# Optimization experiments

Measured on AMD Instinct MI355X. Metric: run time of the kernel, lower is better.

The kernel has to match this reference:

```python
import jax, jax.numpy as jnp
import numpy as np

N, E, D = 50000, 800000, 128   # nodes, edges, input feat dim
H, C = 4, 32                   # heads, per-head channels (H*C = 128)
OUT = 128                      # final linear out_channels
NEG_SLOPE = 0.2


def _glorot(k, shape):
    fan = shape[0] + shape[-1]
    return jax.random.normal(k, shape, jnp.float32) * np.float32(np.sqrt(2.0 / fan))


def setup_inputs() -> dict:
    key = jax.random.key(0)
    ks = jax.random.split(key, 16)
    HC = H * C
    z = lambda n: jnp.zeros((n,), jnp.float32)
    return {
        "x": jax.random.normal(ks[0], (N, D), jnp.float32),
        "edge_index": jax.random.randint(ks[1], (2, E), 0, N),
        "edge_attr": jax.random.uniform(ks[2], (E, 1), jnp.float32),
        # GATv2 layer 1 (in = D)
        "Wl1": _glorot(ks[3], (D, HC)), "bl1": z(HC),
        "Wr1": _glorot(ks[4], (D, HC)), "br1": z(HC),
        "We1": _glorot(ks[5], (1, HC)),
        "att1": _glorot(ks[6], (H, C)),
        "bo1": z(HC),
        # GATv2 layer 2 (in = H*C)
        "Wl2": _glorot(ks[7], (HC, HC)), "bl2": z(HC),
        "Wr2": _glorot(ks[8], (HC, HC)), "br2": z(HC),
        "We2": _glorot(ks[9], (1, HC)),
        "att2": _glorot(ks[10], (H, C)),
        "bo2": z(HC),
        # final Linear
        "Wlin": _glorot(ks[11], (HC, OUT)), "blin": z(OUT),
    }


def _segment_softmax(logits, seg, n):
    # logits: [E_tot, H], seg: [E_tot] target node ids
    m = jax.ops.segment_max(logits, seg, num_segments=n)          # [N, H]
    m = jnp.where(jnp.isfinite(m), m, 0.0)                         # empty-segment guard
    e = jnp.exp(logits - m[seg])
    s = jax.ops.segment_sum(e, seg, num_segments=n)                # [N, H]
    return e / (s[seg] + 1e-16)


def _gatv2_layer(x, src, dst, eattr, Wl, bl, Wr, br, We, att, bo):
    n = x.shape[0]
    xl = (x @ Wl + bl).reshape(n, H, C)   # source transform (lin_l)
    xr = (x @ Wr + br).reshape(n, H, C)   # target transform (lin_r)
    ee = (eattr @ We).reshape(-1, H, C)   # edge transform (lin_edge)
    m = jax.nn.leaky_relu(xl[src] + xr[dst] + ee, NEG_SLOPE)       # [E_tot, H, C]
    logits = jnp.einsum('ehc,hc->eh', m, att)                      # [E_tot, H]
    alpha = _segment_softmax(logits, dst, n)                       # [E_tot, H]
    out = jax.ops.segment_sum(xl[src] * alpha[..., None], dst, num_segments=n)
    return out.reshape(n, H * C) + bo


def _with_self_loops(edge_index, edge_attr, n):
    # PyG add_self_loops(fill_value='mean'): loop attr = mean of incoming edge attrs
    src, dst = edge_index[0], edge_index[1]
    sums = jax.ops.segment_sum(edge_attr, dst, num_segments=n)     # [N, 1]
    cnts = jax.ops.segment_sum(jnp.ones((edge_attr.shape[0], 1), edge_attr.dtype),
                               dst, num_segments=n)
    loop_attr = jnp.where(cnts > 0, sums / jnp.maximum(cnts, 1.0), 0.0)
    ar = jnp.arange(n, dtype=src.dtype)
    full_src = jnp.concatenate([src, ar])
    full_dst = jnp.concatenate([dst, ar])
    full_attr = jnp.concatenate([edge_attr, loop_attr], axis=0)
    return full_src, full_dst, full_attr


def reference(x, edge_index, edge_attr,
              Wl1, bl1, Wr1, br1, We1, att1, bo1,
              Wl2, bl2, Wr2, br2, We2, att2, bo2,
              Wlin, blin):
    x = x.astype(jnp.float32)
    edge_attr = edge_attr.astype(jnp.float32)
    src, dst, eattr = _with_self_loops(edge_index, edge_attr, x.shape[0])
    h = jax.nn.relu(_gatv2_layer(x, src, dst, eattr, Wl1, bl1, Wr1, br1, We1, att1, bo1))
    h = jax.nn.relu(_gatv2_layer(h, src, dst, eattr, Wl2, bl2, Wr2, br2, We2, att2, bo2))
    return jax.nn.relu(h @ Wlin + blin)
```

## Files before the change

kernel.cpp:

```cpp
#include <hip/hip_runtime.h>
#include <hip/hip_fp16.h>
#include <math.h>

#define NEG 0.2f
#define CNT_SHIFT 42
#define SUM_MASK ((1ULL << CNT_SHIFT) - 1)
#define ROWS 48

typedef _Float16 hf2 __attribute__((ext_vector_type(2)));
typedef _Float16 hf8 __attribute__((ext_vector_type(8)));
typedef float f4 __attribute__((ext_vector_type(4)));

template <int CTRL>
__device__ __forceinline__ float dpp_radd(float x) {
  int t = __builtin_amdgcn_update_dpp(0, __float_as_int(x), CTRL, 0xf, 0xf,
                                      false);
  return x + __int_as_float(t);
}

__device__ __forceinline__ uint4 pack_wline(const float* __restrict__ W,
                                            int L) {
  int lane = L & 63, nt = (L >> 6) & 7, kc = L >> 9;
  int kbase = kc * 32 + (lane >> 4) * 8;
  int col = nt * 16 + (lane & 15);
  const float* wp = W + (size_t)kbase * 128 + col;
  uint4 pk;
  pk.x = __builtin_bit_cast(unsigned, __builtin_amdgcn_cvt_pkrtz(wp[0], wp[128]));
  pk.y = __builtin_bit_cast(unsigned, __builtin_amdgcn_cvt_pkrtz(wp[256], wp[384]));
  pk.z = __builtin_bit_cast(unsigned, __builtin_amdgcn_cvt_pkrtz(wp[512], wp[640]));
  pk.w = __builtin_bit_cast(unsigned, __builtin_amdgcn_cvt_pkrtz(wp[768], wp[896]));
  return pk;
}

__global__ __launch_bounds__(256, 2) void k_fuse1(
    const float* __restrict__ X, const float* __restrict__ Wa,
    const float* __restrict__ Wb, const float* __restrict__ Ba,
    const float* __restrict__ Bb, hf2* __restrict__ Y0, hf2* __restrict__ Y1,
    int nrows, int gGemm, const int* __restrict__ ei,
    const float* __restrict__ eattr, unsigned long long* __restrict__ hist,
    unsigned* __restrict__ edge, int E, int nbP,
    const float* __restrict__ W2a, const float* __restrict__ W2b,
    const float* __restrict__ W2c, uint4* __restrict__ wout) {
  __shared__ uint4 Wl[2][1024];
  int bid = blockIdx.x, tid = threadIdx.x;

  if (bid < gGemm) {
    int lane = tid & 63, wid = tid >> 6;
    int quad = lane >> 4, rl = lane & 15;
    int rbase = bid * 128 + wid * 32;

    hf8 a[4][2];
#pragma unroll
    for (int rs = 0; rs < 2; ++rs) {
      int gr = rbase + rs * 16 + rl;
      gr = gr < nrows ? gr : nrows - 1;
      const float* xp = X + (size_t)gr * 128 + quad * 8;
#pragma unroll
      for (int kc = 0; kc < 4; ++kc) {
        float4 u = *reinterpret_cast<const float4*>(xp + kc * 32);
        float4 u2 = *reinterpret_cast<const float4*>(xp + kc * 32 + 4);
        uint4 pk;
        pk.x = __builtin_bit_cast(unsigned, __builtin_amdgcn_cvt_pkrtz(u.x, u.y));
        pk.y = __builtin_bit_cast(unsigned, __builtin_amdgcn_cvt_pkrtz(u.z, u.w));
        pk.z = __builtin_bit_cast(unsigned, __builtin_amdgcn_cvt_pkrtz(u2.x, u2.y));
        pk.w = __builtin_bit_cast(unsigned, __builtin_amdgcn_cvt_pkrtz(u2.z, u2.w));
        a[kc][rs] = __builtin_bit_cast(hf8, pk);
      }
    }

    f4 acc[2][2][8];
#pragma unroll
    for (int m = 0; m < 2; ++m)
#pragma unroll
      for (int rs = 0; rs < 2; ++rs)
#pragma unroll
        for (int nt = 0; nt < 8; ++nt) acc[m][rs][nt] = (f4)0.f;

#pragma unroll
    for (int h = 0; h < 2; ++h) {
      __syncthreads();
#pragma unroll
      for (int m = 0; m < 2; ++m) {
        const float* W = m ? Wb : Wa;
        for (int i = tid; i < 1024; i += 256)
          Wl[m][i] = pack_wline(W, h * 1024 + i);
      }
      __syncthreads();
#pragma unroll
      for (int kcl = 0; kcl < 2; ++kcl) {
        int kc = h * 2 + kcl;
#pragma unroll
        for (int nt = 0; nt < 8; ++nt) {
#pragma unroll
          for (int m = 0; m < 2; ++m) {
            hf8 w = __builtin_bit_cast(hf8,
                Wl[m][(kcl * 8 + nt) * 64 + lane]);
            acc[m][0][nt] = __builtin_amdgcn_mfma_f32_16x16x32_f16(
                w, a[kc][0], acc[m][0][nt], 0, 0, 0);
            acc[m][1][nt] = __builtin_amdgcn_mfma_f32_16x16x32_f16(
                w, a[kc][1], acc[m][1][nt], 0, 0, 0);
          }
        }
      }
    }

#pragma unroll
    for (int m = 0; m < 2; ++m) {
      const float* Bb_ = m ? Bb : Ba;
      hf2* Yv = m ? Y1 : Y0;
#pragma unroll
      for (int rs = 0; rs < 2; ++rs) {
        int row = rbase + rs * 16 + rl;
        if (row < nrows) {
#pragma unroll
          for (int nt = 0; nt < 8; ++nt) {
            f4 av = acc[m][rs][nt];
            int col = nt * 16 + quad * 4;
            float4 bb = *reinterpret_cast<const float4*>(&Bb_[col]);
            float o0 = av[0] + bb.x, o1 = av[1] + bb.y;
            float o2 = av[2] + bb.z, o3 = av[3] + bb.w;
            unsigned p0 = __builtin_bit_cast(unsigned,
                __builtin_amdgcn_cvt_pkrtz(o0, o1));
            unsigned p1 = __builtin_bit_cast(unsigned,
                __builtin_amdgcn_cvt_pkrtz(o2, o3));
            *reinterpret_cast<uint2*>((_Float16*)Yv + (size_t)row * 128 + col)
                = make_uint2(p0, p1);
          }
        }
      }
    }
  } else if (bid < gGemm + nbP) {
    int e0 = (bid - gGemm) * 4096 + tid;
    int d[16], s[16];
    float ea[16];
    bool valid[16];
#pragma unroll
    for (int j = 0; j < 16; ++j) {
      int e = e0 + j * 256;
      valid[j] = e < E;
      int ec = valid[j] ? e : 0;
      d[j] = ei[E + ec];
      s[j] = ei[ec];
      ea[j] = eattr[ec];
    }
#pragma unroll
    for (int j = 0; j < 16; ++j) {
      if (valid[j]) {
        unsigned long long fx =
            (unsigned long long)(ea[j] * 4294967296.0f);
        unsigned long long old =
            atomicAdd(&hist[d[j]], (1ULL << CNT_SHIFT) + fx);
        int rank = (int)(old >> CNT_SHIFT);
        _Float16 h = (_Float16)ea[j];
        unsigned hb = (unsigned)__builtin_bit_cast(unsigned short, h);
        if (rank < ROWS)
          edge[(size_t)d[j] * ROWS + rank] = (unsigned)s[j] | (hb << 16);
      }
    }
  } else {
    int gid = (bid - gGemm - nbP) * 256 + tid;
    if (gid < 3 * 2048) {
      int mat = gid >> 11;
      const float* W = mat == 0 ? W2a : mat == 1 ? W2b : W2c;
      wout[gid] = pack_wline(W, gid & 2047);
    }
  }
}

template <int NMAT, int HALF_OUT>
__global__ __launch_bounds__(256, 2) void k_gemm3(
    const _Float16* __restrict__ X, const uint4* __restrict__ Wp0,
    const uint4* __restrict__ Wp1, const float* __restrict__ B0,
    const float* __restrict__ B1, void* __restrict__ Y0v,
    void* __restrict__ Y1v, int nrows, int dorelu) {
  __shared__ uint4 Wl[NMAT * 2048];
  int tid = threadIdx.x;
  for (int i = tid; i < 2048; i += 256) Wl[i] = Wp0[i];
  if (NMAT == 2)
    for (int i = tid; i < 2048; i += 256) Wl[2048 + i] = Wp1[i];

  int lane = tid & 63, wid = tid >> 6;
  int quad = lane >> 4, rl = lane & 15;
  int rbase = blockIdx.x * 128 + wid * 32;

  hf8 a[4][2];
#pragma unroll
  for (int rs = 0; rs < 2; ++rs) {
    int gr = rbase + rs * 16 + rl;
    gr = gr < nrows ? gr : nrows - 1;
    const _Float16* xp = X + (size_t)gr * 128 + quad * 8;
#pragma unroll
    for (int kc = 0; kc < 4; ++kc)
      a[kc][rs] = *reinterpret_cast<const hf8*>(xp + kc * 32);
  }

  f4 acc[NMAT][2][8];
#pragma unroll
  for (int m = 0; m < NMAT; ++m)
#pragma unroll
    for (int rs = 0; rs < 2; ++rs)
#pragma unroll
      for (int nt = 0; nt < 8; ++nt) acc[m][rs][nt] = (f4)0.f;

  __syncthreads();

#pragma unroll
  for (int kc = 0; kc < 4; ++kc) {
#pragma unroll
    for (int nt = 0; nt < 8; ++nt) {
#pragma unroll
      for (int m = 0; m < NMAT; ++m) {
        hf8 w = __builtin_bit_cast(hf8,
            Wl[m * 2048 + (kc * 8 + nt) * 64 + lane]);
        acc[m][0][nt] = __builtin_amdgcn_mfma_f32_16x16x32_f16(
            w, a[kc][0], acc[m][0][nt], 0, 0, 0);
        acc[m][1][nt] = __builtin_amdgcn_mfma_f32_16x16x32_f16(
            w, a[kc][1], acc[m][1][nt], 0, 0, 0);
      }
    }
  }

#pragma unroll
  for (int m = 0; m < NMAT; ++m) {
    const float* Bb = m ? B1 : B0;
    void* Yv = m ? Y1v : Y0v;
#pragma unroll
    for (int rs = 0; rs < 2; ++rs) {
      int row = rbase + rs * 16 + rl;
      if (row < nrows) {
#pragma unroll
        for (int nt = 0; nt < 8; ++nt) {
          f4 av = acc[m][rs][nt];
          int col = nt * 16 + quad * 4;
          float4 bb = *reinterpret_cast<const float4*>(&Bb[col]);
          float o0 = av[0] + bb.x, o1 = av[1] + bb.y;
          float o2 = av[2] + bb.z, o3 = av[3] + bb.w;
          if (dorelu) {
            o0 = fmaxf(o0, 0.f); o1 = fmaxf(o1, 0.f);
            o2 = fmaxf(o2, 0.f); o3 = fmaxf(o3, 0.f);
          }
          if (HALF_OUT) {
            unsigned p0 = __builtin_bit_cast(unsigned,
                __builtin_amdgcn_cvt_pkrtz(o0, o1));
            unsigned p1 = __builtin_bit_cast(unsigned,
                __builtin_amdgcn_cvt_pkrtz(o2, o3));
            *reinterpret_cast<uint2*>((_Float16*)Yv + (size_t)row * 128 + col)
                = make_uint2(p0, p1);
          } else {
            *reinterpret_cast<float4*>((float*)Yv + (size_t)row * 128 + col)
                = make_float4(o0, o1, o2, o3);
          }
        }
      }
    }
  }
}

__global__ __launch_bounds__(256) void k_gat(const hf2* __restrict__ xl,
    const hf2* __restrict__ xr, const unsigned* __restrict__ edge,
    const unsigned long long* __restrict__ hist, const float* __restrict__ We,
    const float* __restrict__ att, const float* __restrict__ bo,
    hf2* __restrict__ out, int n) {
  int lane = threadIdx.x & 63;
  int wid = threadIdx.x >> 6;
  int v = blockIdx.x * 4 + wid;
  if (v >= n) return;
  int ch = lane * 2;
  hf2 weh = {(_Float16)We[ch], (_Float16)We[ch + 1]};
  hf2 atth = {(_Float16)(att[ch] * 1.44269504f),
              (_Float16)(att[ch + 1] * 1.44269504f)};
  hf2 negh = {(_Float16)NEG, (_Float16)NEG};
  hf2 xrh = xr[(size_t)v * 64 + lane];
  unsigned long long hv = hist[v];
  int cnt = (int)(hv >> CNT_SHIFT);
  int cntc = cnt < ROWS ? cnt : ROWS;
  const unsigned* erow = edge + (size_t)v * ROWS;

  float denom[2] = {0.f, 0.f};
  float ac0[2] = {0.f, 0.f}, ac1[2] = {0.f, 0.f};

  int full = cntc & ~7;
  for (int ofs = 0; ofs < full; ofs += 8) {
    const unsigned* ep = erow + ofs;
    unsigned rec[8];
#pragma unroll
    for (int j = 0; j < 8; ++j) rec[j] = ep[j];
    hf2 xv[8];
#pragma unroll
    for (int j = 0; j < 8; ++j)
      xv[j] = xl[(size_t)(rec[j] & 0xffffu) * 64 + lane];
    float p[8];
#pragma unroll
    for (int j = 0; j < 8; ++j) {
      hf2 eah = __builtin_bit_cast(hf2, (rec[j] >> 16) * 0x10001u);
      hf2 t = (xv[j] + xrh) + eah * weh;
      hf2 tn = t * negh;
      t = __builtin_elementwise_max(t, tn);
      p[j] = __builtin_amdgcn_fdot2(t, atth, 0.f, false);
    }
#pragma unroll
    for (int j = 0; j < 8; ++j) {
      p[j] = dpp_radd<0xB1>(p[j]);
      p[j] = dpp_radd<0x4E>(p[j]);
      p[j] = dpp_radd<0x141>(p[j]);
      p[j] = dpp_radd<0x140>(p[j]);
    }
#pragma unroll
    for (int j = 0; j < 8; ++j) {
      float w = __builtin_amdgcn_exp2f(p[j]);
      denom[j & 1] += w;
      ac0[j & 1] = fmaf(w, (float)xv[j].x, ac0[j & 1]);
      ac1[j & 1] = fmaf(w, (float)xv[j].y, ac1[j & 1]);
    }
  }
  if (full < cntc) {
    const unsigned* ep = erow + full;
    unsigned rec[8];
#pragma unroll
    for (int j = 0; j < 8; ++j) rec[j] = ep[j];
    hf2 xv[8];
#pragma unroll
    for (int j = 0; j < 8; ++j) {
      unsigned si = rec[j] & 0xffffu;
      si = si < (unsigned)n ? si : 0u;
      xv[j] = xl[(size_t)si * 64 + lane];
    }
    float p[8];
#pragma unroll
    for (int j = 0; j < 8; ++j) {
      hf2 eah = __builtin_bit_cast(hf2, (rec[j] >> 16) * 0x10001u);
      hf2 t = (xv[j] + xrh) + eah * weh;
      hf2 tn = t * negh;
      t = __builtin_elementwise_max(t, tn);
      p[j] = __builtin_amdgcn_fdot2(t, atth, 0.f, false);
    }
#pragma unroll
    for (int j = 0; j < 8; ++j) {
      p[j] = dpp_radd<0xB1>(p[j]);
      p[j] = dpp_radd<0x4E>(p[j]);
      p[j] = dpp_radd<0x141>(p[j]);
      p[j] = dpp_radd<0x140>(p[j]);
    }
#pragma unroll
    for (int j = 0; j < 8; ++j) {
      float w = (full + j < cntc) ? __builtin_amdgcn_exp2f(p[j]) : 0.f;
      denom[j & 1] += w;
      ac0[j & 1] = fmaf(w, (float)xv[j].x, ac0[j & 1]);
      ac1[j & 1] = fmaf(w, (float)xv[j].y, ac1[j & 1]);
    }
  }
  {
    float sumf = (float)(hv & SUM_MASK) * 2.3283064365386963e-10f;
    float mean = cnt > 0 ? sumf / (float)cnt : 0.f;
    hf2 xself = xl[(size_t)v * 64 + lane];
    _Float16 mh = (_Float16)mean;
    hf2 meanh = {mh, mh};
    hf2 t = (xself + xrh) + meanh * weh;
    hf2 tn = t * negh;
    t = __builtin_elementwise_max(t, tn);
    float ps = __builtin_amdgcn_fdot2(t, atth, 0.f, false);
    ps = dpp_radd<0xB1>(ps);
    ps = dpp_radd<0x4E>(ps);
    ps = dpp_radd<0x141>(ps);
    ps = dpp_radd<0x140>(ps);
    float w = __builtin_amdgcn_exp2f(ps);
    denom[0] += w;
    ac0[0] = fmaf(w, (float)xself.x, ac0[0]);
    ac1[0] = fmaf(w, (float)xself.y, ac1[0]);
  }
  float rden = 1.0f / (denom[0] + denom[1] + 1e-16f);
  float o0 = fmaxf(fmaf(ac0[0] + ac0[1], rden, bo[ch]), 0.f);
  float o1 = fmaxf(fmaf(ac1[0] + ac1[1], rden, bo[ch + 1]), 0.f);
  hf2 oh = {(_Float16)o0, (_Float16)o1};
  out[(size_t)v * 64 + lane] = oh;
}

extern "C" void kernel_launch(void* const* d_in, const int* in_sizes, int n_in,
                              void* d_out, int out_size, void* d_ws, size_t ws_size,
                              hipStream_t stream) {
  const float* x     = (const float*)d_in[0];
  const int*   ei    = (const int*)d_in[1];
  const float* eattr = (const float*)d_in[2];
  const float* Wl1 = (const float*)d_in[3];
  const float* bl1 = (const float*)d_in[4];
  const float* Wr1 = (const float*)d_in[5];
  const float* br1 = (const float*)d_in[6];
  const float* We1 = (const float*)d_in[7];
  const float* att1 = (const float*)d_in[8];
  const float* bo1 = (const float*)d_in[9];
  const float* Wl2 = (const float*)d_in[10];
  const float* bl2 = (const float*)d_in[11];
  const float* Wr2 = (const float*)d_in[12];
  const float* br2 = (const float*)d_in[13];
  const float* We2 = (const float*)d_in[14];
  const float* att2 = (const float*)d_in[15];
  const float* bo2 = (const float*)d_in[16];
  const float* Wlin = (const float*)d_in[17];
  const float* blin = (const float*)d_in[18];
  float* out = (float*)d_out;

  const int N = in_sizes[0] / 128;
  const int E = in_sizes[1] / 2;

  hf2* xl = (hf2*)d_ws;
  hf2* xr = xl + (size_t)N * 64;
  hf2* h16 = xr + (size_t)N * 64;
  uint4* w16 = (uint4*)(h16 + (size_t)N * 64);
  unsigned long long* hist = (unsigned long long*)(w16 + 3 * 2048);
  unsigned* edge = (unsigned*)(hist + N);

  (void)hipMemsetAsync(hist, 0, sizeof(unsigned long long) * (size_t)N,
                       stream);

  int gGemm = (N + 127) / 128;
  int nbP = (E + 4095) / 4096;
  int gGat = (N + 3) / 4;

  k_fuse1<<<gGemm + nbP + 24, 256, 0, stream>>>(x, Wl1, Wr1, bl1, br1,
      xl, xr, N, gGemm, ei, eattr, hist, edge, E, nbP,
      Wl2, Wr2, Wlin, w16);

  k_gat<<<gGat, 256, 0, stream>>>(xl, xr, edge, hist, We1, att1, bo1, h16, N);

  k_gemm3<2, 1><<<gGemm, 256, 0, stream>>>((const _Float16*)h16,
      w16, w16 + 2048, bl2, br2, xl, xr, N, 0);

  k_gat<<<gGat, 256, 0, stream>>>(xl, xr, edge, hist, We2, att2, bo2, h16, N);

  k_gemm3<1, 0><<<gGemm, 256, 0, stream>>>((const _Float16*)h16,
      w16 + 2 * 2048, nullptr, blin, nullptr, out, nullptr, N, 1);
}
```

Baseline: 276.4 us.

## Distribute edge bucketing via atomic work-stealing chunks across all fused blocks

Measured after the change: 283.0 us. 1.02x slower.

```diff
diff --git a/kernel.cpp b/kernel.cpp
--- a/kernel.cpp
+++ b/kernel.cpp
@@ -38,9 +38,9 @@
     const float* __restrict__ Bb, hf2* __restrict__ Y0, hf2* __restrict__ Y1,
     int nrows, int gGemm, const int* __restrict__ ei,
     const float* __restrict__ eattr, unsigned long long* __restrict__ hist,
-    unsigned* __restrict__ edge, int E, int nbP,
-    const float* __restrict__ W2a, const float* __restrict__ W2b,
-    const float* __restrict__ W2c, uint4* __restrict__ wout) {
+    unsigned* __restrict__ edge, int E, int* __restrict__ cursor,
+    int nChunks, const float* __restrict__ W2a, const float* __restrict__ W2b,
+    const float* __restrict__ W2c, uint4* __restrict__ wout, int nbW) {
   __shared__ uint4 Wl[2][1024];
   int bid = blockIdx.x, tid = threadIdx.x;
 
@@ -129,13 +129,28 @@
         }
       }
     }
-  } else if (bid < gGemm + nbP) {
-    int e0 = (bid - gGemm) * 4096 + tid;
-    int d[16], s[16];
-    float ea[16];
-    bool valid[16];
-#pragma unroll
-    for (int j = 0; j < 16; ++j) {
+  } else if (bid < gGemm + nbW) {
+    int gid = (bid - gGemm) * 256 + tid;
+    if (gid < 3 * 2048) {
+      int mat = gid >> 11;
+      const float* W = mat == 0 ? W2a : mat == 1 ? W2b : W2c;
+      wout[gid] = pack_wline(W, gid & 2047);
+    }
+  }
+
+  for (;;) {
+    __shared__ int chunk_s;
+    if (tid == 0) chunk_s = atomicAdd(cursor, 1);
+    __syncthreads();
+    int chunk = chunk_s;
+    __syncthreads();
+    if (chunk >= nChunks) break;
+    int e0 = chunk * 1024 + tid;
+    int d[4], s[4];
+    float ea[4];
+    bool valid[4];
+#pragma unroll
+    for (int j = 0; j < 4; ++j) {
       int e = e0 + j * 256;
       valid[j] = e < E;
       int ec = valid[j] ? e : 0;
@@ -144,7 +159,7 @@
       ea[j] = eattr[ec];
     }
 #pragma unroll
-    for (int j = 0; j < 16; ++j) {
+    for (int j = 0; j < 4; ++j) {
       if (valid[j]) {
         unsigned long long fx =
             (unsigned long long)(ea[j] * 4294967296.0f);
@@ -156,13 +171,6 @@
         if (rank < ROWS)
           edge[(size_t)d[j] * ROWS + rank] = (unsigned)s[j] | (hb << 16);
       }
-    }
-  } else {
-    int gid = (bid - gGemm - nbP) * 256 + tid;
-    if (gid < 3 * 2048) {
-      int mat = gid >> 11;
-      const float* W = mat == 0 ? W2a : mat == 1 ? W2b : W2c;
-      wout[gid] = pack_wline(W, gid & 2047);
     }
   }
 }
@@ -407,18 +415,21 @@
   hf2* h16 = xr + (size_t)N * 64;
   uint4* w16 = (uint4*)(h16 + (size_t)N * 64);
   unsigned long long* hist = (unsigned long long*)(w16 + 3 * 2048);
-  unsigned* edge = (unsigned*)(hist + N);
-
-  (void)hipMemsetAsync(hist, 0, sizeof(unsigned long long) * (size_t)N,
-                       stream);
+  int* cursor = (int*)(hist + N);
+  unsigned* edge = (unsigned*)(cursor + 4);
+
+  (void)hipMemsetAsync(hist, 0,
+                       sizeof(unsigned long long) * (size_t)N + 16, stream);
 
   int gGemm = (N + 127) / 128;
-  int nbP = (E + 4095) / 4096;
+  int nbW = 24;
+  int nChunks = (E + 1023) / 1024;
+  int nbExtra = 200;
   int gGat = (N + 3) / 4;
 
-  k_fuse1<<<gGemm + nbP + 24, 256, 0, stream>>>(x, Wl1, Wr1, bl1, br1,
-      xl, xr, N, gGemm, ei, eattr, hist, edge, E, nbP,
-      Wl2, Wr2, Wlin, w16);
+  k_fuse1<<<gGemm + nbW + nbExtra, 256, 0, stream>>>(x, Wl1, Wr1, bl1, br1,
+      xl, xr, N, gGemm, ei, eattr, hist, edge, E, cursor, nChunks,
+      Wl2, Wr2, Wlin, w16, nbW);
 
   k_gat<<<gGat, 256, 0, stream>>>(xl, xr, edge, hist, We1, att1, bo1, h16, N);
 
```

## Fuse layer-1 GAT aggregation with layer-2 linear transforms in one kernel

Applied to the files above, without the earlier changes.

New measurement: 271.1 us. Within noise of the previous version (-1.9%).

```diff
diff --git a/kernel.cpp b/kernel.cpp
--- a/kernel.cpp
+++ b/kernel.cpp
@@ -32,244 +32,11 @@
   return pk;
 }
 
-__global__ __launch_bounds__(256, 2) void k_fuse1(
-    const float* __restrict__ X, const float* __restrict__ Wa,
-    const float* __restrict__ Wb, const float* __restrict__ Ba,
-    const float* __restrict__ Bb, hf2* __restrict__ Y0, hf2* __restrict__ Y1,
-    int nrows, int gGemm, const int* __restrict__ ei,
-    const float* __restrict__ eattr, unsigned long long* __restrict__ hist,
-    unsigned* __restrict__ edge, int E, int nbP,
-    const float* __restrict__ W2a, const float* __restrict__ W2b,
-    const float* __restrict__ W2c, uint4* __restrict__ wout) {
-  __shared__ uint4 Wl[2][1024];
-  int bid = blockIdx.x, tid = threadIdx.x;
-
-  if (bid < gGemm) {
-    int lane = tid & 63, wid = tid >> 6;
-    int quad = lane >> 4, rl = lane & 15;
-    int rbase = bid * 128 + wid * 32;
-
-    hf8 a[4][2];
-#pragma unroll
-    for (int rs = 0; rs < 2; ++rs) {
-      int gr = rbase + rs * 16 + rl;
-      gr = gr < nrows ? gr : nrows - 1;
-      const float* xp = X + (size_t)gr * 128 + quad * 8;
-#pragma unroll
-      for (int kc = 0; kc < 4; ++kc) {
-        float4 u = *reinterpret_cast<const float4*>(xp + kc * 32);
-        float4 u2 = *reinterpret_cast<const float4*>(xp + kc * 32 + 4);
-        uint4 pk;
-        pk.x = __builtin_bit_cast(unsigned, __builtin_amdgcn_cvt_pkrtz(u.x, u.y));
-        pk.y = __builtin_bit_cast(unsigned, __builtin_amdgcn_cvt_pkrtz(u.z, u.w));
-        pk.z = __builtin_bit_cast(unsigned, __builtin_amdgcn_cvt_pkrtz(u2.x, u2.y));
-        pk.w = __builtin_bit_cast(unsigned, __builtin_amdgcn_cvt_pkrtz(u2.z, u2.w));
-        a[kc][rs] = __builtin_bit_cast(hf8, pk);
-      }
-    }
-
-    f4 acc[2][2][8];
-#pragma unroll
-    for (int m = 0; m < 2; ++m)
-#pragma unroll
-      for (int rs = 0; rs < 2; ++rs)
-#pragma unroll
-        for (int nt = 0; nt < 8; ++nt) acc[m][rs][nt] = (f4)0.f;
-
-#pragma unroll
-    for (int h = 0; h < 2; ++h) {
-      __syncthreads();
-#pragma unroll
-      for (int m = 0; m < 2; ++m) {
-        const float* W = m ? Wb : Wa;
-        for (int i = tid; i < 1024; i += 256)
-          Wl[m][i] = pack_wline(W, h * 1024 + i);
-      }
-      __syncthreads();
-#pragma unroll
-      for (int kcl = 0; kcl < 2; ++kcl) {
-        int kc = h * 2 + kcl;
-#pragma unroll
-        for (int nt = 0; nt < 8; ++nt) {
-#pragma unroll
-          for (int m = 0; m < 2; ++m) {
-            hf8 w = __builtin_bit_cast(hf8,
-                Wl[m][(kcl * 8 + nt) * 64 + lane]);
-            acc[m][0][nt] = __builtin_amdgcn_mfma_f32_16x16x32_f16(
-                w, a[kc][0], acc[m][0][nt], 0, 0, 0);
-            acc[m][1][nt] = __builtin_amdgcn_mfma_f32_16x16x32_f16(
-                w, a[kc][1], acc[m][1][nt], 0, 0, 0);
-          }
-        }
-      }
-    }
-
-#pragma unroll
-    for (int m = 0; m < 2; ++m) {
-      const float* Bb_ = m ? Bb : Ba;
-      hf2* Yv = m ? Y1 : Y0;
-#pragma unroll
-      for (int rs = 0; rs < 2; ++rs) {
-        int row = rbase + rs * 16 + rl;
-        if (row < nrows) {
-#pragma unroll
-          for (int nt = 0; nt < 8; ++nt) {
-            f4 av = acc[m][rs][nt];
-            int col = nt * 16 + quad * 4;
-            float4 bb = *reinterpret_cast<const float4*>(&Bb_[col]);
-            float o0 = av[0] + bb.x, o1 = av[1] + bb.y;
-            float o2 = av[2] + bb.z, o3 = av[3] + bb.w;
-            unsigned p0 = __builtin_bit_cast(unsigned,
-                __builtin_amdgcn_cvt_pkrtz(o0, o1));
-            unsigned p1 = __builtin_bit_cast(unsigned,
-                __builtin_amdgcn_cvt_pkrtz(o2, o3));
-            *reinterpret_cast<uint2*>((_Float16*)Yv + (size_t)row * 128 + col)
-                = make_uint2(p0, p1);
-          }
-        }
-      }
-    }
-  } else if (bid < gGemm + nbP) {
-    int e0 = (bid - gGemm) * 4096 + tid;
-    int d[16], s[16];
-    float ea[16];
-    bool valid[16];
-#pragma unroll
-    for (int j = 0; j < 16; ++j) {
-      int e = e0 + j * 256;
-      valid[j] = e < E;
-      int ec = valid[j] ? e : 0;
-      d[j] = ei[E + ec];
-      s[j] = ei[ec];
-      ea[j] = eattr[ec];
-    }
-#pragma unroll
-    for (int j = 0; j < 16; ++j) {
-      if (valid[j]) {
-        unsigned long long fx =
-            (unsigned long long)(ea[j] * 4294967296.0f);
-        unsigned long long old =
-            atomicAdd(&hist[d[j]], (1ULL << CNT_SHIFT) + fx);
-        int rank = (int)(old >> CNT_SHIFT);
-        _Float16 h = (_Float16)ea[j];
-        unsigned hb = (unsigned)__builtin_bit_cast(unsigned short, h);
-        if (rank < ROWS)
-          edge[(size_t)d[j] * ROWS + rank] = (unsigned)s[j] | (hb << 16);
-      }
-    }
-  } else {
-    int gid = (bid - gGemm - nbP) * 256 + tid;
-    if (gid < 3 * 2048) {
-      int mat = gid >> 11;
-      const float* W = mat == 0 ? W2a : mat == 1 ? W2b : W2c;
-      wout[gid] = pack_wline(W, gid & 2047);
-    }
-  }
-}
-
-template <int NMAT, int HALF_OUT>
-__global__ __launch_bounds__(256, 2) void k_gemm3(
-    const _Float16* __restrict__ X, const uint4* __restrict__ Wp0,
-    const uint4* __restrict__ Wp1, const float* __restrict__ B0,
-    const float* __restrict__ B1, void* __restrict__ Y0v,
-    void* __restrict__ Y1v, int nrows, int dorelu) {
-  __shared__ uint4 Wl[NMAT * 2048];
-  int tid = threadIdx.x;
-  for (int i = tid; i < 2048; i += 256) Wl[i] = Wp0[i];
-  if (NMAT == 2)
-    for (int i = tid; i < 2048; i += 256) Wl[2048 + i] = Wp1[i];
-
-  int lane = tid & 63, wid = tid >> 6;
-  int quad = lane >> 4, rl = lane & 15;
-  int rbase = blockIdx.x * 128 + wid * 32;
-
-  hf8 a[4][2];
-#pragma unroll
-  for (int rs = 0; rs < 2; ++rs) {
-    int gr = rbase + rs * 16 + rl;
-    gr = gr < nrows ? gr : nrows - 1;
-    const _Float16* xp = X + (size_t)gr * 128 + quad * 8;
-#pragma unroll
-    for (int kc = 0; kc < 4; ++kc)
-      a[kc][rs] = *reinterpret_cast<const hf8*>(xp + kc * 32);
-  }
-
-  f4 acc[NMAT][2][8];
-#pragma unroll
-  for (int m = 0; m < NMAT; ++m)
-#pragma unroll
-    for (int rs = 0; rs < 2; ++rs)
-#pragma unroll
-      for (int nt = 0; nt < 8; ++nt) acc[m][rs][nt] = (f4)0.f;
-
-  __syncthreads();
-
-#pragma unroll
-  for (int kc = 0; kc < 4; ++kc) {
-#pragma unroll
-    for (int nt = 0; nt < 8; ++nt) {
-#pragma unroll
-      for (int m = 0; m < NMAT; ++m) {
-        hf8 w = __builtin_bit_cast(hf8,
-            Wl[m * 2048 + (kc * 8 + nt) * 64 + lane]);
-        acc[m][0][nt] = __builtin_amdgcn_mfma_f32_16x16x32_f16(
-            w, a[kc][0], acc[m][0][nt], 0, 0, 0);
-        acc[m][1][nt] = __builtin_amdgcn_mfma_f32_16x16x32_f16(
-            w, a[kc][1], acc[m][1][nt], 0, 0, 0);
-      }
-    }
-  }
-
-#pragma unroll
-  for (int m = 0; m < NMAT; ++m) {
-    const float* Bb = m ? B1 : B0;
-    void* Yv = m ? Y1v : Y0v;
-#pragma unroll
-    for (int rs = 0; rs < 2; ++rs) {
-      int row = rbase + rs * 16 + rl;
-      if (row < nrows) {
-#pragma unroll
-        for (int nt = 0; nt < 8; ++nt) {
-          f4 av = acc[m][rs][nt];
-          int col = nt * 16 + quad * 4;
-          float4 bb = *reinterpret_cast<const float4*>(&Bb[col]);
-          float o0 = av[0] + bb.x, o1 = av[1] + bb.y;
-          float o2 = av[2] + bb.z, o3 = av[3] + bb.w;
-          if (dorelu) {
-            o0 = fmaxf(o0, 0.f); o1 = fmaxf(o1, 0.f);
-            o2 = fmaxf(o2, 0.f); o3 = fmaxf(o3, 0.f);
-          }
-          if (HALF_OUT) {
-            unsigned p0 = __builtin_bit_cast(unsigned,
-                __builtin_amdgcn_cvt_pkrtz(o0, o1));
-            unsigned p1 = __builtin_bit_cast(unsigned,
-                __builtin_amdgcn_cvt_pkrtz(o2, o3));
-            *reinterpret_cast<uint2*>((_Float16*)Yv + (size_t)row * 128 + col)
-                = make_uint2(p0, p1);
-          } else {
-            *reinterpret_cast<float4*>((float*)Yv + (size_t)row * 128 + col)
-                = make_float4(o0, o1, o2, o3);
-          }
-        }
-      }
-    }
-  }
-}
-
-__global__ __launch_bounds__(256) void k_gat(const hf2* __restrict__ xl,
+__device__ __forceinline__ hf2 gat_node(int v, const hf2* __restrict__ xl,
     const hf2* __restrict__ xr, const unsigned* __restrict__ edge,
-    const unsigned long long* __restrict__ hist, const float* __restrict__ We,
-    const float* __restrict__ att, const float* __restrict__ bo,
-    hf2* __restrict__ out, int n) {
-  int lane = threadIdx.x & 63;
-  int wid = threadIdx.x >> 6;
-  int v = blockIdx.x * 4 + wid;
-  if (v >= n) return;
+    const unsigned long long* __restrict__ hist, hf2 weh, hf2 atth, hf2 negh,
+    const float* __restrict__ bo, int lane, int n) {
   int ch = lane * 2;
-  hf2 weh = {(_Float16)We[ch], (_Float16)We[ch + 1]};
-  hf2 atth = {(_Float16)(att[ch] * 1.44269504f),
-              (_Float16)(att[ch + 1] * 1.44269504f)};
-  hf2 negh = {(_Float16)NEG, (_Float16)NEG};
   hf2 xrh = xr[(size_t)v * 64 + lane];
   unsigned long long hv = hist[v];
   int cnt = (int)(hv >> CNT_SHIFT);
@@ -369,10 +136,291 @@
     ac1[0] = fmaf(w, (float)xself.y, ac1[0]);
   }
   float rden = 1.0f / (denom[0] + denom[1] + 1e-16f);
-  float o0 = fmaxf(fmaf(ac0[0] + ac0[1], rden, bo[ch]), 0.f);
-  float o1 = fmaxf(fmaf(ac1[0] + ac1[1], rden, bo[ch + 1]), 0.f);
+  int ch0 = ch;
+  float o0 = fmaxf(fmaf(ac0[0] + ac0[1], rden, bo[ch0]), 0.f);
+  float o1 = fmaxf(fmaf(ac1[0] + ac1[1], rden, bo[ch0 + 1]), 0.f);
   hf2 oh = {(_Float16)o0, (_Float16)o1};
+  return oh;
+}
+
+__global__ __launch_bounds__(256, 2) void k_fuse1(
+    const float* __restrict__ X, const float* __restrict__ Wa,
+    const float* __restrict__ Wb, const float* __restrict__ Ba,
+    const float* __restrict__ Bb, hf2* __restrict__ Y0, hf2* __restrict__ Y1,
+    int nrows, int gGemm, const int* __restrict__ ei,
+    const float* __restrict__ eattr, unsigned long long* __restrict__ hist,
+    unsigned* __restrict__ edge, int E, int nbP,
+    const float* __restrict__ W2a, const float* __restrict__ W2b,
+    const float* __restrict__ W2c, uint4* __restrict__ wout) {
+  __shared__ uint4 Wl[2][1024];
+  int bid = blockIdx.x, tid = threadIdx.x;
+
+  if (bid < gGemm) {
+    int lane = tid & 63, wid = tid >> 6;
+    int quad = lane >> 4, rl = lane & 15;
+    int rbase = bid * 128 + wid * 32;
+
+    hf8 a[4][2];
+#pragma unroll
+    for (int rs = 0; rs < 2; ++rs) {
+      int gr = rbase + rs * 16 + rl;
+      gr = gr < nrows ? gr : nrows - 1;
+      const float* xp = X + (size_t)gr * 128 + quad * 8;
+#pragma unroll
+      for (int kc = 0; kc < 4; ++kc) {
+        float4 u = *reinterpret_cast<const float4*>(xp + kc * 32);
+        float4 u2 = *reinterpret_cast<const float4*>(xp + kc * 32 + 4);
+        uint4 pk;
+        pk.x = __builtin_bit_cast(unsigned, __builtin_amdgcn_cvt_pkrtz(u.x, u.y));
+        pk.y = __builtin_bit_cast(unsigned, __builtin_amdgcn_cvt_pkrtz(u.z, u.w));
+        pk.z = __builtin_bit_cast(unsigned, __builtin_amdgcn_cvt_pkrtz(u2.x, u2.y));
+        pk.w = __builtin_bit_cast(unsigned, __builtin_amdgcn_cvt_pkrtz(u2.z, u2.w));
+        a[kc][rs] = __builtin_bit_cast(hf8, pk);
+      }
+    }
+
+    f4 acc[2][2][8];
+#pragma unroll
+    for (int m = 0; m < 2; ++m)
+#pragma unroll
+      for (int rs = 0; rs < 2; ++rs)
+#pragma unroll
+        for (int nt = 0; nt < 8; ++nt) acc[m][rs][nt] = (f4)0.f;
+
+#pragma unroll
+    for (int h = 0; h < 2; ++h) {
+      __syncthreads();
+#pragma unroll
+      for (int m = 0; m < 2; ++m) {
+        const float* W = m ? Wb : Wa;
+        for (int i = tid; i < 1024; i += 256)
+          Wl[m][i] = pack_wline(W, h * 1024 + i);
+      }
+      __syncthreads();
+#pragma unroll
+      for (int kcl = 0; kcl < 2; ++kcl) {
+        int kc = h * 2 + kcl;
+#pragma unroll
+        for (int nt = 0; nt < 8; ++nt) {
+#pragma unroll
+          for (int m = 0; m < 2; ++m) {
+            hf8 w = __builtin_bit_cast(hf8,
+                Wl[m][(kcl * 8 + nt) * 64 + lane]);
+            acc[m][0][nt] = __builtin_amdgcn_mfma_f32_16x16x32_f16(
+                w, a[kc][0], acc[m][0][nt], 0, 0, 0);
+            acc[m][1][nt] = __builtin_amdgcn_mfma_f32_16x16x32_f16(
+                w, a[kc][1], acc[m][1][nt], 0, 0, 0);
+          }
+        }
+      }
+    }
+
+#pragma unroll
+    for (int m = 0; m < 2; ++m) {
+      const float* Bb_ = m ? Bb : Ba;
+      hf2* Yv = m ? Y1 : Y0;
+#pragma unroll
+      for (int rs = 0; rs < 2; ++rs) {
+        int row = rbase + rs * 16 + rl;
+        if (row < nrows) {
+#pragma unroll
+          for (int nt = 0; nt < 8; ++nt) {
+            f4 av = acc[m][rs][nt];
+            int col = nt * 16 + quad * 4;
+            float4 bb = *reinterpret_cast<const float4*>(&Bb_[col]);
+            float o0 = av[0] + bb.x, o1 = av[1] + bb.y;
+            float o2 = av[2] + bb.z, o3 = av[3] + bb.w;
+            unsigned p0 = __builtin_bit_cast(unsigned,
+                __builtin_amdgcn_cvt_pkrtz(o0, o1));
+            unsigned p1 = __builtin_bit_cast(unsigned,
+                __builtin_amdgcn_cvt_pkrtz(o2, o3));
+            *reinterpret_cast<uint2*>((_Float16*)Yv + (size_t)row * 128 + col)
+                = make_uint2(p0, p1);
+          }
+        }
+      }
+    }
+  } else if (bid < gGemm + nbP) {
+    int e0 = (bid - gGemm) * 4096 + tid;
+    int d[16], s[16];
+    float ea[16];
+    bool valid[16];
+#pragma unroll
+    for (int j = 0; j < 16; ++j) {
+      int e = e0 + j * 256;
+      valid[j] = e < E;
+      int ec = valid[j] ? e : 0;
+      d[j] = ei[E + ec];
+      s[j] = ei[ec];
+      ea[j] = eattr[ec];
+    }
+#pragma unroll
+    for (int j = 0; j < 16; ++j) {
+      if (valid[j]) {
+        unsigned long long fx =
+            (unsigned long long)(ea[j] * 4294967296.0f);
+        unsigned long long old =
+            atomicAdd(&hist[d[j]], (1ULL << CNT_SHIFT) + fx);
+        int rank = (int)(old >> CNT_SHIFT);
+        _Float16 h = (_Float16)ea[j];
+        unsigned hb = (unsigned)__builtin_bit_cast(unsigned short, h);
+        if (rank < ROWS)
+          edge[(size_t)d[j] * ROWS + rank] = (unsigned)s[j] | (hb << 16);
+      }
+    }
+  } else {
+    int gid = (bid - gGemm - nbP) * 256 + tid;
+    if (gid < 3 * 2048) {
+      int mat = gid >> 11;
+      const float* W = mat == 0 ? W2a : mat == 1 ? W2b : W2c;
+      wout[gid] = pack_wline(W, gid & 2047);
+    }
+  }
+}
+
+__global__ __launch_bounds__(256) void k_gatg(const hf2* __restrict__ xl,
+    const hf2* __restrict__ xr, const unsigned* __restrict__ edge,
+    const unsigned long long* __restrict__ hist, const float* __restrict__ We,
+    const float* __restrict__ att, const float* __restrict__ bo,
+    const uint4* __restrict__ Wp0, const uint4* __restrict__ Wp1,
+    const float* __restrict__ B0, const float* __restrict__ B1,
+    hf2* __restrict__ out0, hf2* __restrict__ out1, int n) {
+  __shared__ _Float16 hbuf[16][136];
+  int tid = threadIdx.x;
+  int lane = tid & 63, wid = tid >> 6;
+  int quad = lane >> 4, rl = lane & 15;
+  int base = blockIdx.x * 16;
+  int ch = lane * 2;
+  hf2 weh = {(_Float16)We[ch], (_Float16)We[ch + 1]};
+  hf2 atth = {(_Float16)(att[ch] * 1.44269504f),
+              (_Float16)(att[ch + 1] * 1.44269504f)};
+  hf2 negh = {(_Float16)NEG, (_Float16)NEG};
+
+#pragma unroll 1
+  for (int i = 0; i < 4; ++i) {
+    int row = wid * 4 + i;
+    int v = base + row;
+    hf2 oh = {(_Float16)0.f, (_Float16)0.f};
+    if (v < n)
+      oh = gat_node(v, xl, xr, edge, hist, weh, atth, negh, bo, lane, n);
+    *reinterpret_cast<hf2*>(&hbuf[row][2 * lane]) = oh;
+  }
+  __syncthreads();
+
+  hf8 hfrag[4];
+#pragma unroll
+  for (int kc = 0; kc < 4; ++kc)
+    hfrag[kc] = *reinterpret_cast<const hf8*>(&hbuf[rl][kc * 32 + quad * 8]);
+
+#pragma unroll
+  for (int ntl = 0; ntl < 2; ++ntl) {
+    int nt = wid * 2 + ntl;
+#pragma unroll
+    for (int m = 0; m < 2; ++m) {
+      const uint4* Wp = m ? Wp1 : Wp0;
+      f4 a = (f4)0.f;
+#pragma unroll
+      for (int kc = 0; kc < 4; ++kc) {
+        hf8 w = __builtin_bit_cast(hf8, Wp[(kc * 8 + nt) * 64 + lane]);
+        a = __builtin_amdgcn_mfma_f32_16x16x32_f16(w, hfrag[kc], a, 0, 0, 0);
+      }
+      int col = nt * 16 + quad * 4;
+      const float* Bb = m ? B1 : B0;
+      float4 bb = *reinterpret_cast<const float4*>(&Bb[col]);
+      float o0 = a[0] + bb.x, o1 = a[1] + bb.y;
+      float o2 = a[2] + bb.z, o3 = a[3] + bb.w;
+      hf2 h0 = {(_Float16)o0, (_Float16)o1};
+      hf2 h1 = {(_Float16)o2, (_Float16)o3};
+      int row = base + rl;
+      if (row < n) {
+        hf2* outp = m ? out1 : out0;
+        uint2 pk = make_uint2(__builtin_bit_cast(unsigned, h0),
+                              __builtin_bit_cast(unsigned, h1));
+        *reinterpret_cast<uint2*>(outp + (size_t)row * 64 + nt * 8 + quad * 2)
+            = pk;
+      }
+    }
+  }
+}
+
+__global__ __launch_bounds__(256) void k_gat(const hf2* __restrict__ xl,
+    const hf2* __restrict__ xr, const unsigned* __restrict__ edge,
+    const unsigned long long* __restrict__ hist, const float* __restrict__ We,
+    const float* __restrict__ att, const float* __restrict__ bo,
+    hf2* __restrict__ out, int n) {
+  int lane = threadIdx.x & 63;
+  int wid = threadIdx.x >> 6;
+  int v = blockIdx.x * 4 + wid;
+  if (v >= n) return;
+  int ch = lane * 2;
+  hf2 weh = {(_Float16)We[ch], (_Float16)We[ch + 1]};
+  hf2 atth = {(_Float16)(att[ch] * 1.44269504f),
+              (_Float16)(att[ch + 1] * 1.44269504f)};
+  hf2 negh = {(_Float16)NEG, (_Float16)NEG};
+  hf2 oh = gat_node(v, xl, xr, edge, hist, weh, atth, negh, bo, lane, n);
   out[(size_t)v * 64 + lane] = oh;
+}
+
+__global__ __launch_bounds__(256, 2) void k_gemmf(
+    const _Float16* __restrict__ X, const uint4* __restrict__ Wp0,
+    const float* __restrict__ B0, float* __restrict__ Y, int nrows) {
+  __shared__ uint4 Wl[2048];
+  int tid = threadIdx.x;
+  for (int i = tid; i < 2048; i += 256) Wl[i] = Wp0[i];
+
+  int lane = tid & 63, wid = tid >> 6;
+  int quad = lane >> 4, rl = lane & 15;
+  int rbase = blockIdx.x * 128 + wid * 32;
+
+  hf8 a[4][2];
+#pragma unroll
+  for (int rs = 0; rs < 2; ++rs) {
+    int gr = rbase + rs * 16 + rl;
+    gr = gr < nrows ? gr : nrows - 1;
+    const _Float16* xp = X + (size_t)gr * 128 + quad * 8;
+#pragma unroll
+    for (int kc = 0; kc < 4; ++kc)
+      a[kc][rs] = *reinterpret_cast<const hf8*>(xp + kc * 32);
+  }
+
+  f4 acc[2][8];
+#pragma unroll
+  for (int rs = 0; rs < 2; ++rs)
+#pragma unroll
+    for (int nt = 0; nt < 8; ++nt) acc[rs][nt] = (f4)0.f;
+
+  __syncthreads();
+
+#pragma unroll
+  for (int kc = 0; kc < 4; ++kc) {
+#pragma unroll
+    for (int nt = 0; nt < 8; ++nt) {
+      hf8 w = __builtin_bit_cast(hf8, Wl[(kc * 8 + nt) * 64 + lane]);
+      acc[0][nt] = __builtin_amdgcn_mfma_f32_16x16x32_f16(
+          w, a[kc][0], acc[0][nt], 0, 0, 0);
+      acc[1][nt] = __builtin_amdgcn_mfma_f32_16x16x32_f16(
+          w, a[kc][1], acc[1][nt], 0, 0, 0);
+    }
+  }
+
+#pragma unroll
+  for (int rs = 0; rs < 2; ++rs) {
+    int row = rbase + rs * 16 + rl;
+    if (row < nrows) {
+#pragma unroll
+      for (int nt = 0; nt < 8; ++nt) {
+        f4 av = acc[rs][nt];
+        int col = nt * 16 + quad * 4;
+        float4 bb = *reinterpret_cast<const float4*>(&B0[col]);
+        float o0 = fmaxf(av[0] + bb.x, 0.f);
+        float o1 = fmaxf(av[1] + bb.y, 0.f);
+        float o2 = fmaxf(av[2] + bb.z, 0.f);
+        float o3 = fmaxf(av[3] + bb.w, 0.f);
+        *reinterpret_cast<float4*>(&Y[(size_t)row * 128 + col]) =
+            make_float4(o0, o1, o2, o3);
+      }
+    }
+  }
 }
 
 extern "C" void kernel_launch(void* const* d_in, const int* in_sizes, int n_in,
@@ -409,24 +457,27 @@
   unsigned long long* hist = (unsigned long long*)(w16 + 3 * 2048);
   unsigned* edge = (unsigned*)(hist + N);
 
+  hf2* xl2 = (hf2*)d_out;
+  hf2* xr2 = xl2 + (size_t)N * 64;
+
   (void)hipMemsetAsync(hist, 0, sizeof(unsigned long long) * (size_t)N,
                        stream);
 
   int gGemm = (N + 127) / 128;
   int nbP = (E + 4095) / 4096;
   int gGat = (N + 3) / 4;
+  int gGatg = (N + 15) / 16;
 
   k_fuse1<<<gGemm + nbP + 24, 256, 0, stream>>>(x, Wl1, Wr1, bl1, br1,
       xl, xr, N, gGemm, ei, eattr, hist, edge, E, nbP,
       Wl2, Wr2, Wlin, w16);
 
-  k_gat<<<gGat, 256, 0, stream>>>(xl, xr, edge, hist, We1, att1, bo1, h16, N);
-
-  k_gemm3<2, 1><<<gGemm, 256, 0, stream>>>((const _Float16*)h16,
-      w16, w16 + 2048, bl2, br2, xl, xr, N, 0);
-
-  k_gat<<<gGat, 256, 0, stream>>>(xl, xr, edge, hist, We2, att2, bo2, h16, N);
-
-  k_gemm3<1, 0><<<gGemm, 256, 0, stream>>>((const _Float16*)h16,
-      w16 + 2 * 2048, nullptr, blin, nullptr, out, nullptr, N, 1);
-}
+  k_gatg<<<gGatg, 256, 0, stream>>>(xl, xr, edge, hist, We1, att1, bo1,
+      w16, w16 + 2048, bl2, br2, xl2, xr2, N);
+
+  k_gat<<<gGat, 256, 0, stream>>>(xl2, xr2, edge, hist, We2, att2, bo2,
+                                  h16, N);
+
+  k_gemmf<<<gGemm, 256, 0, stream>>>((const _Float16*)h16, w16 + 2 * 2048,
+                                     blin, out, N);
+}
```
